# Optimization experiments

Hardware: AMD Instinct MI355X
Metric: run time of the kernel (lower is better)

Reference implementation:

```python
import jax, jax.numpy as jnp
import numpy as np

B, N, H, A, S = 8, 8192, 256, 64, 32  # batch, nodes, hidden, annotation, sub_graphs


def _mysoftmax(x):
    # exp, zero out where x <= 0, normalize over last dim, nan (0/0) -> 0
    x_exp = jnp.where(x > 0, jnp.exp(x), 0.0)
    part = jnp.sum(x_exp, axis=-1, keepdims=True)
    # safe divide: where partition == 0 the faithful result after nan_to_num is 0
    return jnp.where(part > 0, x_exp / jnp.where(part > 0, part, 1.0), 0.0)


def setup_inputs() -> dict:
    key = jax.random.key(0)
    k1, k2, k3, k4, k5, k6 = jax.random.split(key, 6)
    x = jax.random.normal(k1, (B, N, H + A), dtype=jnp.float32)
    node_map = jax.random.uniform(k2, (B, S, N), dtype=jnp.float32)
    lim = 1.0 / np.sqrt(H + A)
    Wi = jax.random.uniform(k3, (H, H + A), minval=-lim, maxval=lim, dtype=jnp.float32)
    bi = jax.random.uniform(k4, (H,), minval=-lim, maxval=lim, dtype=jnp.float32)
    Wj = jax.random.uniform(k5, (H, H + A), minval=-lim, maxval=lim, dtype=jnp.float32)
    bj = jax.random.uniform(k6, (H,), minval=-lim, maxval=lim, dtype=jnp.float32)
    return {"x": x, "node_map": node_map, "Wi": Wi, "bi": bi, "Wj": Wj, "bj": bj}


def reference(x, node_map, Wi, bi, Wj, bj):
    # gated node features: sigmoid(fc_i(x)) * tanh(fc_j(x))  -> [B, N, H]
    x_sigm = jax.nn.sigmoid(jnp.einsum('bnf,hf->bnh', x, Wi) + bi)
    x_tanh = jnp.tanh(jnp.einsum('bnf,hf->bnh', x, Wj) + bj)
    x_all = x_sigm * x_tanh
    # per-node L2 norm -> [B, 1, N]
    x_norm = jnp.linalg.norm(x_all, axis=-1)[:, None, :]
    # scaled subgraph map and masked softmax over nodes -> [B, S, N]
    weight = _mysoftmax(node_map * x_norm)
    # weighted sum over nodes (replaces [B,S,N,H] broadcast) -> [B, S, H]
    pooled = jnp.einsum('bsn,bnh->bsh', weight, x_all)
    return jnp.tanh(pooled), weight[..., None]
```

## Files before the change

### kernel.cpp

```cpp
#include <hip/hip_runtime.h>
#include <cstdint>
#include <cstddef>

typedef unsigned short u16;
typedef unsigned int   u32;
using short8 = __attribute__((ext_vector_type(8))) short;
using f32x4  = __attribute__((ext_vector_type(4))) float;

#define NB    8
#define NN    8192
#define HH    256
#define FF    320
#define SS    32
#define NROWS 65536
#define NCH   32

__device__ __forceinline__ u16 f2bf(float f) {
    union { float f; u32 u; } v; v.f = f;
    u32 r = v.u + 0x7fffu + ((v.u >> 16) & 1u);
    return (u16)(r >> 16);
}
__device__ __forceinline__ u32 pk2(float a, float b) {
    return (u32)f2bf(a) | ((u32)f2bf(b) << 16);
}
__device__ __forceinline__ short8 pack8(float4 a, float4 b) {
    union { u32 u[4]; short8 s; } r;
    r.u[0] = pk2(a.x, a.y); r.u[1] = pk2(a.z, a.w);
    r.u[2] = pk2(b.x, b.y); r.u[3] = pk2(b.z, b.w);
    return r.s;
}

__global__ __launch_bounds__(256) void prep_w(const float* __restrict__ Wi,
                                              const float* __restrict__ Wj,
                                              u16* __restrict__ Wb,
                                              float* __restrict__ normsq) {
    int idx = blockIdx.x * 256 + threadIdx.x;
    float v = (idx < 81920) ? Wi[idx] : Wj[idx - 81920];
    Wb[idx] = f2bf(v);
    if (idx < NROWS) normsq[idx] = 0.f;
}

__global__ __launch_bounds__(512, 4) void gemm_gate(
    const float* __restrict__ x, const u16* __restrict__ Wb,
    const float* __restrict__ bi, const float* __restrict__ bj,
    u16* __restrict__ xa, float* __restrict__ normsq)
{
    __shared__ u16 lB[5 * 8192];

    const int bx   = blockIdx.x;
    const int xcd  = bx & 7;
    const int ht   = (bx >> 3) & 3;
    const int slot = bx >> 5;
    const int mb   = xcd + slot * 8;
    const int m0   = mb * 256;
    const int h0   = ht * 64;
    const int b_idx = m0 >> 13;
    const int n0    = m0 & 8191;

    const int tid  = threadIdx.x;
    const int w    = tid >> 6;
    const int lane = tid & 63;
    const int quad = lane >> 4;
    const int l15  = lane & 15;

    {
        const int rsub = lane >> 3;
        const int kg   = (lane & 7) ^ rsub;
        #pragma unroll
        for (int kt = 0; kt < 5; ++kt) {
            #pragma unroll
            for (int j = 0; j < 2; ++j) {
                int sl  = w * 2 + j;
                int row = sl * 8 + rsub;
                int mat = row >> 6, hl = row & 63;
                const u16* gsrc = Wb + mat * 81920 + (size_t)(h0 + hl) * FF + kt * 64 + kg * 8;
                u16* ldst = &lB[kt * 8192 + sl * 512];
                __builtin_amdgcn_global_load_lds(
                    (const __attribute__((address_space(1))) void*)gsrc,
                    (__attribute__((address_space(3))) void*)ldst, 16, 0, 0);
            }
        }
    }

    const float* xb = x + (size_t)(m0 + w * 32 + l15) * FF + quad * 8;

    f32x4 acc[8][2];
    #pragma unroll
    for (int a = 0; a < 8; ++a)
        #pragma unroll
        for (int m = 0; m < 2; ++m) acc[a][m] = (f32x4){0.f, 0.f, 0.f, 0.f};

    float4 pre[2][2][2];
    #pragma unroll
    for (int mt = 0; mt < 2; ++mt) {
        pre[0][mt][0] = *reinterpret_cast<const float4*>(xb + mt * 16 * FF);
        pre[0][mt][1] = *reinterpret_cast<const float4*>(xb + mt * 16 * FF + 4);
    }

    __syncthreads();

    #pragma unroll
    for (int kt = 0; kt < 5; ++kt) {
        #pragma unroll
        for (int kk = 0; kk < 2; ++kk) {
            const int ks  = kt * 2 + kk;
            const int cur = ks & 1, nxt = cur ^ 1;
            if (ks < 9) {
                const int f = (ks + 1) * 32;
                #pragma unroll
                for (int mt = 0; mt < 2; ++mt) {
                    pre[nxt][mt][0] = *reinterpret_cast<const float4*>(xb + mt * 16 * FF + f);
                    pre[nxt][mt][1] = *reinterpret_cast<const float4*>(xb + mt * 16 * FF + f + 4);
                }
            }
            short8 af[2];
            #pragma unroll
            for (int mt = 0; mt < 2; ++mt)
                af[mt] = pack8(pre[cur][mt][0], pre[cur][mt][1]);
            #pragma unroll
            for (int mn = 0; mn < 8; ++mn) {
                int c = mn * 16 + l15;
                short8 bv = *reinterpret_cast<const short8*>(
                    &lB[kt * 8192 + c * 64 + (((kk * 4 + quad) ^ (c & 7)) << 3)]);
                acc[mn][0] = __builtin_amdgcn_mfma_f32_16x16x32_bf16(af[0], bv, acc[mn][0], 0, 0, 0);
                acc[mn][1] = __builtin_amdgcn_mfma_f32_16x16x32_bf16(af[1], bv, acc[mn][1], 0, 0, 0);
            }
        }
    }

    float s0[2][4];
    #pragma unroll
    for (int mt = 0; mt < 2; ++mt)
        #pragma unroll
        for (int r = 0; r < 4; ++r) s0[mt][r] = 0.f;

    #pragma unroll
    for (int hq = 0; hq < 4; ++hq) {
        int h = h0 + hq * 16 + l15;
        float bi_v = bi[h], bj_v = bj[h];
        #pragma unroll
        for (int mt = 0; mt < 2; ++mt) {
            float xall[4];
            #pragma unroll
            for (int r = 0; r < 4; ++r) {
                float yi = acc[hq][mt][r] + bi_v;
                float yj = acc[hq + 4][mt][r] + bj_v;
                float sg = 1.f / (1.f + __expf(-yi));
                float e2 = __expf(-2.f * yj);
                float th = (1.f - e2) / (1.f + e2);
                float xv = sg * th;
                xall[r] = xv;
                s0[mt][r] += xv * xv;
            }
            uint2 pk;
            pk.x = pk2(xall[0], xall[1]);
            pk.y = pk2(xall[2], xall[3]);
            size_t o = (size_t)b_idx * ((size_t)HH * NN) + (size_t)h * NN
                     + (size_t)(n0 + w * 32 + mt * 16 + quad * 4);
            *reinterpret_cast<uint2*>(&xa[o]) = pk;
        }
    }
    #pragma unroll
    for (int m = 1; m <= 8; m <<= 1) {
        #pragma unroll
        for (int mt = 0; mt < 2; ++mt)
            #pragma unroll
            for (int r = 0; r < 4; ++r)
                s0[mt][r] += __shfl_xor(s0[mt][r], m, 64);
    }
    if (l15 == 0) {
        #pragma unroll
        for (int mt = 0; mt < 2; ++mt)
            #pragma unroll
            for (int r = 0; r < 4; ++r)
                atomicAdd(&normsq[m0 + w * 32 + mt * 16 + quad * 4 + r], s0[mt][r]);
    }
}

__global__ __launch_bounds__(1024) void softmax_k(
    const float* __restrict__ nm, const float* __restrict__ normsq,
    float* __restrict__ out1)
{
    __shared__ float red[16];
    int bs = blockIdx.x;
    int b  = bs >> 5;
    const float* src = nm + (size_t)bs * NN;
    float* dst       = out1 + (size_t)bs * NN;
    const float* ns  = normsq + (size_t)b * NN;
    int tid = threadIdx.x;
    float e[8];
    float sum = 0.f;
    #pragma unroll
    for (int i = 0; i < 8; ++i) {
        int n = i * 1024 + tid;
        float logit = src[n] * sqrtf(ns[n]);
        float v = (logit > 0.f) ? __expf(logit) : 0.f;
        e[i] = v;
        sum += v;
    }
    #pragma unroll
    for (int m = 1; m <= 32; m <<= 1) sum += __shfl_xor(sum, m, 64);
    int w = tid >> 6, lane = tid & 63;
    if (lane == 0) red[w] = sum;
    __syncthreads();
    float part = 0.f;
    #pragma unroll
    for (int j = 0; j < 16; ++j) part += red[j];
    float inv = (part > 0.f) ? (1.f / part) : 0.f;
    #pragma unroll
    for (int i = 0; i < 8; ++i) dst[i * 1024 + tid] = e[i] * inv;
}

__global__ __launch_bounds__(256) void pooled_k(
    const u16* __restrict__ xa, const float* __restrict__ wgt,
    float* __restrict__ part)
{
    __shared__ u16 lw[32 * 264];
    int bx = blockIdx.x;
    int b  = bx >> 5, c = bx & 31;
    int n0 = c * 256;
    int tid = threadIdx.x, w = tid >> 6, lane = tid & 63, quad = lane >> 4, l15 = lane & 15;

    {
        int s  = tid >> 3;
        int nb = (tid & 7) * 32;
        const float* src = wgt + (size_t)(b * SS + s) * NN + n0 + nb;
        #pragma unroll
        for (int q = 0; q < 8; ++q) {
            float4 v = *reinterpret_cast<const float4*>(src + q * 4);
            uint2 pk;
            pk.x = pk2(v.x, v.y);
            pk.y = pk2(v.z, v.w);
            *reinterpret_cast<uint2*>(&lw[s * 264 + nb + q * 4]) = pk;
        }
    }
    __syncthreads();

    f32x4 acc[4][2];
    #pragma unroll
    for (int a = 0; a < 4; ++a)
        #pragma unroll
        for (int s = 0; s < 2; ++s) acc[a][s] = (f32x4){0.f, 0.f, 0.f, 0.f};

    const u16* ab = xa + (size_t)b * ((size_t)HH * NN) + n0;
    #pragma unroll
    for (int ks = 0; ks < 8; ++ks) {
        short8 av[4];
        #pragma unroll
        for (int htl = 0; htl < 4; ++htl) {
            int h = w * 64 + htl * 16 + l15;
            av[htl] = *reinterpret_cast<const short8*>(ab + (size_t)h * NN + ks * 32 + quad * 8);
        }
        #pragma unroll
        for (int st = 0; st < 2; ++st) {
            int s = st * 16 + l15;
            short8 bv = *reinterpret_cast<const short8*>(&lw[s * 264 + ks * 32 + quad * 8]);
            #pragma unroll
            for (int htl = 0; htl < 4; ++htl)
                acc[htl][st] = __builtin_amdgcn_mfma_f32_16x16x32_bf16(av[htl], bv, acc[htl][st], 0, 0, 0);
        }
    }
    float* pb = part + (size_t)(b * NCH + c) * 8192;
    #pragma unroll
    for (int htl = 0; htl < 4; ++htl) {
        #pragma unroll
        for (int st = 0; st < 2; ++st) {
            int h = w * 64 + htl * 16 + quad * 4;
            int s = st * 16 + l15;
            *reinterpret_cast<f32x4*>(&pb[s * 256 + h]) = acc[htl][st];
        }
    }
}

__global__ __launch_bounds__(256) void reduce_tanh(const float* __restrict__ part,
                                                   float* __restrict__ out0)
{
    int gid = blockIdx.x * 256 + threadIdx.x;
    int b = gid >> 13, r = gid & 8191;
    const float* p = part + (size_t)b * NCH * 8192 + r;
    float s = 0.f;
    #pragma unroll
    for (int c = 0; c < NCH; ++c) s += p[(size_t)c * 8192];
    out0[gid] = tanhf(s);
}

extern "C" void kernel_launch(void* const* d_in, const int* in_sizes, int n_in,
                              void* d_out, int out_size, void* d_ws, size_t ws_size,
                              hipStream_t stream) {
    const float* x  = (const float*)d_in[0];
    const float* nm = (const float*)d_in[1];
    const float* Wi = (const float*)d_in[2];
    const float* bi = (const float*)d_in[3];
    const float* Wj = (const float*)d_in[4];
    const float* bj = (const float*)d_in[5];
    float* out0 = (float*)d_out;
    float* out1 = out0 + NB * SS * HH;

    char* ws = (char*)d_ws;
    u16*   Wb     = (u16*)ws;
    u16*   xa     = (u16*)(ws + 327680);
    float* normsq = (float*)(ws + 327680 + 33554432);
    float* part   = (float*)(ws + 327680 + 33554432 + 262144);

    prep_w     <<<640,  256, 0, stream>>>(Wi, Wj, Wb, normsq);
    gemm_gate  <<<1024, 512, 0, stream>>>(x, Wb, bi, bj, xa, normsq);
    softmax_k  <<<256, 1024, 0, stream>>>(nm, normsq, out1);
    pooled_k   <<<256,  256, 0, stream>>>(xa, out1, part);
    reduce_tanh<<<256,  256, 0, stream>>>(part, out0);
}
```

Before: 199.9 us.

## Split pooled kernel into more node chunks and deepen load prefetching

Doubles the number of node chunks in the pooling GEMM so it launches twice as many blocks, each with a double-buffered prefetch of xa tiles. The gate GEMM gets a three-stage register prefetch for x. The fp32-to-bf16 packing becomes a cheaper round-half-up using a byte permute. The trade-offs are more partial sums for the reduction step, more registers, and slightly different rounding.

```diff
diff --git a/kernel.cpp b/kernel.cpp
--- a/kernel.cpp
+++ b/kernel.cpp
@@ -13,20 +13,21 @@
 #define FF    320
 #define SS    32
 #define NROWS 65536
-#define NCH   32
+#define NCH   64
 
 __device__ __forceinline__ u16 f2bf(float f) {
     union { float f; u32 u; } v; v.f = f;
     u32 r = v.u + 0x7fffu + ((v.u >> 16) & 1u);
     return (u16)(r >> 16);
 }
-__device__ __forceinline__ u32 pk2(float a, float b) {
-    return (u32)f2bf(a) | ((u32)f2bf(b) << 16);
+__device__ __forceinline__ u32 pk2h(float lo, float hi) {
+    union { float f; u32 u; } a, b; a.f = lo; b.f = hi;
+    return __builtin_amdgcn_perm(b.u + 0x8000u, a.u + 0x8000u, 0x07060302u);
 }
 __device__ __forceinline__ short8 pack8(float4 a, float4 b) {
     union { u32 u[4]; short8 s; } r;
-    r.u[0] = pk2(a.x, a.y); r.u[1] = pk2(a.z, a.w);
-    r.u[2] = pk2(b.x, b.y); r.u[3] = pk2(b.z, b.w);
+    r.u[0] = pk2h(a.x, a.y); r.u[1] = pk2h(a.z, a.w);
+    r.u[2] = pk2h(b.x, b.y); r.u[3] = pk2h(b.z, b.w);
     return r.s;
 }
 
@@ -90,41 +91,39 @@
         #pragma unroll
         for (int m = 0; m < 2; ++m) acc[a][m] = (f32x4){0.f, 0.f, 0.f, 0.f};
 
-    float4 pre[2][2][2];
-    #pragma unroll
-    for (int mt = 0; mt < 2; ++mt) {
-        pre[0][mt][0] = *reinterpret_cast<const float4*>(xb + mt * 16 * FF);
-        pre[0][mt][1] = *reinterpret_cast<const float4*>(xb + mt * 16 * FF + 4);
-    }
+    float4 pre[3][2][2];
+    #pragma unroll
+    for (int s = 0; s < 2; ++s)
+        #pragma unroll
+        for (int mt = 0; mt < 2; ++mt) {
+            pre[s][mt][0] = *reinterpret_cast<const float4*>(xb + mt * 16 * FF + s * 32);
+            pre[s][mt][1] = *reinterpret_cast<const float4*>(xb + mt * 16 * FF + s * 32 + 4);
+        }
 
     __syncthreads();
 
     #pragma unroll
-    for (int kt = 0; kt < 5; ++kt) {
-        #pragma unroll
-        for (int kk = 0; kk < 2; ++kk) {
-            const int ks  = kt * 2 + kk;
-            const int cur = ks & 1, nxt = cur ^ 1;
-            if (ks < 9) {
-                const int f = (ks + 1) * 32;
-                #pragma unroll
-                for (int mt = 0; mt < 2; ++mt) {
-                    pre[nxt][mt][0] = *reinterpret_cast<const float4*>(xb + mt * 16 * FF + f);
-                    pre[nxt][mt][1] = *reinterpret_cast<const float4*>(xb + mt * 16 * FF + f + 4);
-                }
+    for (int ks = 0; ks < 10; ++ks) {
+        const int kt  = ks >> 1, kk = ks & 1;
+        const int cur = ks % 3;
+        if (ks < 8) {
+            const int nx = (ks + 2) % 3;
+            const int f  = (ks + 2) * 32;
+            #pragma unroll
+            for (int mt = 0; mt < 2; ++mt) {
+                pre[nx][mt][0] = *reinterpret_cast<const float4*>(xb + mt * 16 * FF + f);
+                pre[nx][mt][1] = *reinterpret_cast<const float4*>(xb + mt * 16 * FF + f + 4);
             }
-            short8 af[2];
-            #pragma unroll
-            for (int mt = 0; mt < 2; ++mt)
-                af[mt] = pack8(pre[cur][mt][0], pre[cur][mt][1]);
-            #pragma unroll
-            for (int mn = 0; mn < 8; ++mn) {
-                int c = mn * 16 + l15;
-                short8 bv = *reinterpret_cast<const short8*>(
-                    &lB[kt * 8192 + c * 64 + (((kk * 4 + quad) ^ (c & 7)) << 3)]);
-                acc[mn][0] = __builtin_amdgcn_mfma_f32_16x16x32_bf16(af[0], bv, acc[mn][0], 0, 0, 0);
-                acc[mn][1] = __builtin_amdgcn_mfma_f32_16x16x32_bf16(af[1], bv, acc[mn][1], 0, 0, 0);
-            }
+        }
+        short8 af0 = pack8(pre[cur][0][0], pre[cur][0][1]);
+        short8 af1 = pack8(pre[cur][1][0], pre[cur][1][1]);
+        #pragma unroll
+        for (int mn = 0; mn < 8; ++mn) {
+            int c = mn * 16 + l15;
+            short8 bv = *reinterpret_cast<const short8*>(
+                &lB[kt * 8192 + c * 64 + (((kk * 4 + quad) ^ (c & 7)) << 3)]);
+            acc[mn][0] = __builtin_amdgcn_mfma_f32_16x16x32_bf16(af0, bv, acc[mn][0], 0, 0, 0);
+            acc[mn][1] = __builtin_amdgcn_mfma_f32_16x16x32_bf16(af1, bv, acc[mn][1], 0, 0, 0);
         }
     }
 
@@ -153,8 +152,8 @@
                 s0[mt][r] += xv * xv;
             }
             uint2 pk;
-            pk.x = pk2(xall[0], xall[1]);
-            pk.y = pk2(xall[2], xall[3]);
+            pk.x = pk2h(xall[0], xall[1]);
+            pk.y = pk2h(xall[2], xall[3]);
             size_t o = (size_t)b_idx * ((size_t)HH * NN) + (size_t)h * NN
                      + (size_t)(n0 + w * 32 + mt * 16 + quad * 4);
             *reinterpret_cast<uint2*>(&xa[o]) = pk;
@@ -215,23 +214,32 @@
     const u16* __restrict__ xa, const float* __restrict__ wgt,
     float* __restrict__ part)
 {
-    __shared__ u16 lw[32 * 264];
+    __shared__ u16 lw[32 * 136];
     int bx = blockIdx.x;
-    int b  = bx >> 5, c = bx & 31;
-    int n0 = c * 256;
+    int b  = bx >> 6, c = bx & 63;
+    int n0 = c * 128;
     int tid = threadIdx.x, w = tid >> 6, lane = tid & 63, quad = lane >> 4, l15 = lane & 15;
+
+    const u16* ab = xa + (size_t)b * ((size_t)HH * NN) + n0;
+
+    short8 av[2][4];
+    #pragma unroll
+    for (int htl = 0; htl < 4; ++htl) {
+        int h = w * 64 + htl * 16 + l15;
+        av[0][htl] = *reinterpret_cast<const short8*>(ab + (size_t)h * NN + quad * 8);
+    }
 
     {
         int s  = tid >> 3;
-        int nb = (tid & 7) * 32;
-        const float* src = wgt + (size_t)(b * SS + s) * NN + n0 + nb;
-        #pragma unroll
-        for (int q = 0; q < 8; ++q) {
+        int jq = (tid & 7) * 16;
+        const float* src = wgt + (size_t)(b * SS + s) * NN + n0 + jq;
+        #pragma unroll
+        for (int q = 0; q < 4; ++q) {
             float4 v = *reinterpret_cast<const float4*>(src + q * 4);
             uint2 pk;
-            pk.x = pk2(v.x, v.y);
-            pk.y = pk2(v.z, v.w);
-            *reinterpret_cast<uint2*>(&lw[s * 264 + nb + q * 4]) = pk;
+            pk.x = pk2h(v.x, v.y);
+            pk.y = pk2h(v.z, v.w);
+            *reinterpret_cast<uint2*>(&lw[s * 136 + jq + q * 4]) = pk;
         }
     }
     __syncthreads();
@@ -242,22 +250,24 @@
         #pragma unroll
         for (int s = 0; s < 2; ++s) acc[a][s] = (f32x4){0.f, 0.f, 0.f, 0.f};
 
-    const u16* ab = xa + (size_t)b * ((size_t)HH * NN) + n0;
-    #pragma unroll
-    for (int ks = 0; ks < 8; ++ks) {
-        short8 av[4];
-        #pragma unroll
-        for (int htl = 0; htl < 4; ++htl) {
-            int h = w * 64 + htl * 16 + l15;
-            av[htl] = *reinterpret_cast<const short8*>(ab + (size_t)h * NN + ks * 32 + quad * 8);
+    #pragma unroll
+    for (int ks = 0; ks < 4; ++ks) {
+        const int cur = ks & 1, nxt = cur ^ 1;
+        if (ks < 3) {
+            #pragma unroll
+            for (int htl = 0; htl < 4; ++htl) {
+                int h = w * 64 + htl * 16 + l15;
+                av[nxt][htl] = *reinterpret_cast<const short8*>(
+                    ab + (size_t)h * NN + (ks + 1) * 32 + quad * 8);
+            }
         }
         #pragma unroll
         for (int st = 0; st < 2; ++st) {
             int s = st * 16 + l15;
-            short8 bv = *reinterpret_cast<const short8*>(&lw[s * 264 + ks * 32 + quad * 8]);
+            short8 bv = *reinterpret_cast<const short8*>(&lw[s * 136 + ks * 32 + quad * 8]);
             #pragma unroll
             for (int htl = 0; htl < 4; ++htl)
-                acc[htl][st] = __builtin_amdgcn_mfma_f32_16x16x32_bf16(av[htl], bv, acc[htl][st], 0, 0, 0);
+                acc[htl][st] = __builtin_amdgcn_mfma_f32_16x16x32_bf16(av[cur][htl], bv, acc[htl][st], 0, 0, 0);
         }
     }
     float* pb = part + (size_t)(b * NCH + c) * 8192;
@@ -305,6 +315,6 @@
     prep_w     <<<640,  256, 0, stream>>>(Wi, Wj, Wb, normsq);
     gemm_gate  <<<1024, 512, 0, stream>>>(x, Wb, bi, bj, xa, normsq);
     softmax_k  <<<256, 1024, 0, stream>>>(nm, normsq, out1);
-    pooled_k   <<<256,  256, 0, stream>>>(xa, out1, part);
+    pooled_k   <<<512,  256, 0, stream>>>(xa, out1, part);
     reduce_tanh<<<256,  256, 0, stream>>>(part, out0);
 }
```

New measurement: 214.9 us. +7.5%, slower.
